# Kernel optimization log

Hardware: AMD Instinct MI355X
Metric: run time of the kernel (lower is better)

The kernel has to match this reference:

```python
import jax, jax.numpy as jnp
import numpy as np

N, E = 20000, 640000
D_IN, D_H, D_OUT = 128, 64, 32


def _lin_w(key, out_d, in_d):
    return jax.random.normal(key, (out_d, in_d), jnp.float32) / np.sqrt(in_d)


def setup_inputs() -> dict:
    key = jax.random.key(0)
    ks = jax.random.split(key, 16)
    x = jax.random.normal(ks[0], (N, D_IN), jnp.float32)
    edge_index = jax.random.randint(ks[1], (2, E), 0, N, jnp.int64)
    inp = {"x": x, "edge_index": edge_index}
    # SAGEConv weights: lin_l (aggregated neighbors, with bias), lin_r (root, no bias)
    inp["Wl1"] = _lin_w(ks[2], D_H, D_IN); inp["bl1"] = jnp.zeros((D_H,), jnp.float32)
    inp["Wr1"] = _lin_w(ks[3], D_H, D_IN)
    inp["Wl2"] = _lin_w(ks[4], D_H, D_H); inp["bl2"] = jnp.zeros((D_H,), jnp.float32)
    inp["Wr2"] = _lin_w(ks[5], D_H, D_H)
    inp["Wl3"] = _lin_w(ks[6], D_OUT, D_H); inp["bl3"] = jnp.zeros((D_OUT,), jnp.float32)
    inp["Wr3"] = _lin_w(ks[7], D_OUT, D_H)
    # Conv2d kernels (OIHW), all 3x3 pad 1
    inp["Wc1"] = jax.random.normal(ks[8], (D_H, 1, 3, 3), jnp.float32) / 3.0
    inp["bc1"] = jnp.zeros((D_H,), jnp.float32)
    inp["Wc2"] = jax.random.normal(ks[9], (D_H, D_H, 3, 3), jnp.float32) / np.sqrt(9 * D_H)
    inp["bc2"] = jnp.zeros((D_H,), jnp.float32)
    inp["Wc3"] = jax.random.normal(ks[10], (1, D_H, 3, 3), jnp.float32) / np.sqrt(9 * D_H)
    inp["bc3"] = jnp.zeros((1,), jnp.float32)
    # linear2 (hidden -> hidden)
    inp["W2"] = _lin_w(ks[11], D_H, D_H); inp["b2"] = jnp.zeros((D_H,), jnp.float32)
    return inp


def _sage(x, src, dst, Wl, bl, Wr):
    # PyG SAGEConv (mean aggr): lin_l(mean_{j->i} x_j) + lin_r(x_i)
    msg = x[src]  # [E, d] gather
    agg = jax.ops.segment_sum(msg, dst, num_segments=N)
    deg = jax.ops.segment_sum(jnp.ones((src.shape[0], 1), x.dtype), dst, num_segments=N)
    agg = agg / jnp.maximum(deg, 1.0)
    return agg @ Wl.T + bl + x @ Wr.T


def _conv(x, w, b):
    y = jax.lax.conv_general_dilated(x, w, (1, 1), ((1, 1), (1, 1)),
                                     dimension_numbers=("NCHW", "OIHW", "NCHW"))
    return y + b[None, :, None, None]


def reference(x, edge_index, Wl1, bl1, Wr1, Wl2, bl2, Wr2, Wl3, bl3, Wr3,
              Wc1, bc1, Wc2, bc2, Wc3, bc3, W2, b2):
    src, dst = edge_index[0], edge_index[1]
    h = _sage(x, src, dst, Wl1, bl1, Wr1)
    h = _sage(h, src, dst, Wl2, bl2, Wr2)
    h = _sage(h, src, dst, Wl2, bl2, Wr2)  # sage2 reused, as in source
    out_1 = h
    h4 = h[None, None]                     # [1,1,N,D_H]
    out = _conv(h4, Wc1, bc1)              # [1,D_H,N,D_H]
    out = _conv(out, Wc2, bc2)             # dropout is identity at inference
    out = _conv(out, Wc3, bc3)             # [1,1,N,D_H]
    out = out[0, 0] + out_1
    out = out @ W2.T + b2
    h = _sage(out, src, dst, Wl2, bl2, Wr2)
    h = _sage(h, src, dst, Wl2, bl2, Wr2)
    h = _sage(h, src, dst, Wl3, bl3, Wr3)
    return h
```

## Files before the change

### kernel.cpp

```cpp
#include <hip/hip_runtime.h>

#define NN 20000
#define NE 640000
#define NBUK 79

__global__ __launch_bounds__(128) void k_init(const int* __restrict__ ei32,
                                              int* __restrict__ bins,
                                              int* __restrict__ flag) {
  int tid = threadIdx.x;
  if (tid < NBUK) bins[tid] = 0;
  if (tid < 64) {
    int v = ei32[2 * tid + 1];
    unsigned long long nz = __ballot(v != 0);
    if (tid == 0) *flag = (nz == 0ull) ? 2 : 1;
  }
}

__global__ __launch_bounds__(256) void k_histB(const int* __restrict__ ei,
                                               const int* __restrict__ flag,
                                               int* __restrict__ bins, int E) {
  __shared__ int lb[NBUK];
  int tid = threadIdx.x;
  for (int i = tid; i < NBUK; i += 256) lb[i] = 0;
  __syncthreads();
  int st = *flag;
  int e0 = blockIdx.x * 4096;
#pragma unroll
  for (int t = 0; t < 16; ++t) {
    int e = e0 + t * 256 + tid;
    if (e < E) atomicAdd(&lb[ei[(size_t)(E + e) * st] >> 8], 1);
  }
  __syncthreads();
  for (int i = tid; i < NBUK; i += 256)
    if (lb[i]) atomicAdd(&bins[i], lb[i]);
}

__global__ __launch_bounds__(128) void k_scan79(const int* __restrict__ bins,
                                                int* __restrict__ bbase,
                                                int* __restrict__ bcur,
                                                int* __restrict__ rowptr,
                                                int E, int N) {
  __shared__ int lds[128];
  int tid = threadIdx.x;
  int mine = (tid < NBUK) ? bins[tid] : 0;
  lds[tid] = mine;
  __syncthreads();
  for (int off = 1; off < 128; off <<= 1) {
    int v = (tid >= off) ? lds[tid - off] : 0;
    __syncthreads();
    lds[tid] += v;
    __syncthreads();
  }
  int ex = lds[tid] - mine;
  if (tid <= NBUK) {
    bbase[tid] = ex;
    if (tid < NBUK) bcur[tid] = ex;
  }
  if (tid == 0) rowptr[N] = E;
}

__global__ __launch_bounds__(256) void k_part(const int* __restrict__ ei,
                                              const int* __restrict__ flag,
                                              int* __restrict__ bcur,
                                              unsigned long long* __restrict__ ebuf,
                                              int E) {
  __shared__ int lcnt[NBUK];
  __shared__ int lbase[NBUK];
  int tid = threadIdx.x;
  for (int i = tid; i < NBUK; i += 256) lcnt[i] = 0;
  __syncthreads();
  int st = *flag;
  int e0 = blockIdx.x * 4096;
  int srcv[16], dstv[16], lrank[16], bk[16];
  int n = 0;
#pragma unroll
  for (int t = 0; t < 16; ++t) {
    int e = e0 + t * 256 + tid;
    if (e < E) {
      int s = ei[(size_t)e * st];
      int d = ei[(size_t)(E + e) * st];
      int b = d >> 8;
      srcv[n] = s; dstv[n] = d; bk[n] = b;
      lrank[n] = atomicAdd(&lcnt[b], 1);
      ++n;
    }
  }
  __syncthreads();
  for (int i = tid; i < NBUK; i += 256)
    lbase[i] = atomicAdd(&bcur[i], lcnt[i]);
  __syncthreads();
  for (int t = 0; t < n; ++t) {
    int pos = lbase[bk[t]] + lrank[t];
    ebuf[pos] = ((unsigned long long)(unsigned)dstv[t] << 32) | (unsigned)srcv[t];
  }
}

__global__ __launch_bounds__(256) void k_sortb(
    const unsigned long long* __restrict__ ebuf, const int* __restrict__ bbase,
    int* __restrict__ rowptr, float* __restrict__ invdeg,
    int* __restrict__ csr, int N) {
  __shared__ int lcnt[256];
  __shared__ int lcur[256];
  __shared__ int wsum[4];
  int b = blockIdx.x;
  int tid = threadIdx.x;
  int base = bbase[b], n = bbase[b + 1] - base;
  lcnt[tid] = 0;
  __syncthreads();
  for (int e = tid; e < n; e += 256) {
    int d = (int)(ebuf[base + e] >> 32);
    atomicAdd(&lcnt[d - (b << 8)], 1);
  }
  __syncthreads();
  int c = lcnt[tid];
  int lane = tid & 63, wid = tid >> 6;
  int s = c;
#pragma unroll
  for (int off = 1; off < 64; off <<= 1) {
    int v = __shfl_up(s, off, 64);
    if (lane >= off) s += v;
  }
  if (lane == 63) wsum[wid] = s;
  __syncthreads();
  int woff = 0;
  for (int w = 0; w < wid; ++w) woff += wsum[w];
  int pref = woff + s - c;
  int gnode = (b << 8) + tid;
  if (gnode < N) {
    rowptr[gnode] = base + pref;
    invdeg[gnode] = 1.0f / (float)(c < 1 ? 1 : c);
  }
  lcur[tid] = pref;
  __syncthreads();
  for (int e = tid; e < n; e += 256) {
    unsigned long long pk = ebuf[base + e];
    int d = (int)(pk >> 32);
    int pos = atomicAdd(&lcur[d - (b << 8)], 1);
    csr[base + pos] = (int)(unsigned)pk;
  }
}

__global__ __launch_bounds__(256) void k_wtransA(
    const float* __restrict__ Wl1, const float* __restrict__ Wr1,
    const float* __restrict__ Wl2, const float* __restrict__ Wr2,
    const float* __restrict__ Wl3, const float* __restrict__ Wr3,
    const float* __restrict__ W2,
    float* __restrict__ Wt1, float* __restrict__ Wt2,
    float* __restrict__ Wt3, float* __restrict__ W2t) {
  int idx = blockIdx.x * 256 + threadIdx.x;
  if (idx < 16384) {
    int w = idx >> 7, u = idx & 127;
    Wt1[idx] = (u < 64) ? Wl1[u * 128 + w] : Wr1[(u - 64) * 128 + w];
  } else if (idx < 24576) {
    int t = idx - 16384;
    int w = t >> 7, u = t & 127;
    Wt2[t] = (u < 64) ? Wl2[u * 64 + w] : Wr2[(u - 64) * 64 + w];
  } else if (idx < 28672) {
    int t = idx - 24576;
    int w = t >> 6, u = t & 63;
    Wt3[t] = (u < 32) ? Wl3[u * 64 + w] : Wr3[(u - 32) * 64 + w];
  } else {
    int t = idx - 28672;
    int w = t >> 6, u = t & 63;
    W2t[t] = W2[u * 64 + w];
  }
}

__device__ __forceinline__ bool maskB(int var, int o2, int o1) {
  int s = o2 + o1;
  switch (var) {
    case 0: return (o2 >= 0) && (s >= 0);
    case 1: return s >= -1;
    case 3: return s <= 1;
    case 4: return (o2 <= 0) && (s <= 0);
    default: return true;
  }
}

__global__ __launch_bounds__(256) void k_setup2(
    const float* __restrict__ Wc1, const float* __restrict__ Wc2,
    const float* __restrict__ Wc3, const float* __restrict__ bc1,
    const float* __restrict__ bc2, const float* __restrict__ bc3,
    const float* __restrict__ W2t, const float* __restrict__ Wt2,
    const float* __restrict__ b2,
    float* __restrict__ T729, float* __restrict__ beta5,
    float* __restrict__ Wf, float* __restrict__ bf) {
  int b = blockIdx.x, tid = threadIdx.x;
  if (b == 0) {
    __shared__ float W3[576];
    __shared__ float S9s[5184];
    __shared__ float W1s[576];
    for (int e = tid; e < 576; e += 256) { W3[e] = Wc3[e]; W1s[e] = Wc1[e]; }
    __syncthreads();
    for (int bb = tid; bb < 576; bb += 256) {
      float acc[9];
#pragma unroll
      for (int a = 0; a < 9; ++a) acc[a] = 0.0f;
#pragma unroll 4
      for (int o = 0; o < 64; ++o) {
        float w2 = Wc2[o * 576 + bb];
#pragma unroll
        for (int a = 0; a < 9; ++a) acc[a] += W3[o * 9 + a] * w2;
      }
#pragma unroll
      for (int a = 0; a < 9; ++a) S9s[a * 576 + bb] = acc[a];
    }
    __syncthreads();
    for (int c = tid; c < 729; c += 256) {
      int kx0  = c % 3;
      int dl1e = (c / 3) % 3;
      int dl2e = (c / 9) % 3;
      int ky0  = (c / 27) % 3;
      int ky1  = (c / 81) % 3;
      int ky2  = c / 243;
      const float* s9 = &S9s[(ky2 * 3 + dl2e) * 576 + ky1 * 3 + dl1e];
      const float* w1 = &W1s[ky0 * 3 + kx0];
      float t = 0.0f;
#pragma unroll 8
      for (int i = 0; i < 64; ++i) t += s9[i * 9] * w1[i * 9];
      T729[c] = t;
    }
  } else if (b <= 5) {
    __shared__ float S2[576];
    __shared__ float W3b[576];
    __shared__ float B2[64];
    __shared__ float part[256];
    int var = b - 1;
    for (int e = tid; e < 576; e += 256) {
      int o = e / 9, r = e - o * 9;
      float t = 0.0f;
      for (int i = 0; i < 64; ++i) t += Wc2[o * 576 + i * 9 + r] * bc1[i];
      S2[e] = t;
      W3b[e] = Wc3[e];
    }
    if (tid < 64) B2[tid] = bc2[tid];
    __syncthreads();
    int u = tid & 63, oc = tid >> 6;
    float s = 0.0f;
    for (int ky2 = 0; ky2 < 3; ++ky2) {
      int o2 = ky2 - 1;
      bool okA = (var == 0) ? (o2 >= 0) : (var == 4) ? (o2 <= 0) : true;
      if (!okA) continue;
      for (int dl2 = -1; dl2 <= 1; ++dl2) {
        int p = u + dl2; if ((unsigned)p >= 64u) continue;
        float sel[9];
#pragma unroll
        for (int ky1 = 0; ky1 < 3; ++ky1) {
          int o1 = ky1 - 1;
          bool mb = maskB(var, o2, o1);
#pragma unroll
          for (int dl1 = -1; dl1 <= 1; ++dl1) {
            int pq = p + dl1;
            sel[ky1 * 3 + dl1 + 1] = (mb && (unsigned)pq < 64u) ? 1.0f : 0.0f;
          }
        }
#pragma unroll 4
        for (int oo = 0; oo < 16; ++oo) {
          int o = oc * 16 + oo;
          float inner = B2[o];
#pragma unroll
          for (int r = 0; r < 9; ++r) inner += S2[o * 9 + r] * sel[r];
          s += W3b[o * 9 + ky2 * 3 + (dl2 + 1)] * inner;
        }
      }
    }
    part[tid] = s;
    __syncthreads();
    if (tid < 64) {
      beta5[var * 64 + tid] =
          bc3[0] + part[tid] + part[64 + tid] + part[128 + tid] + part[192 + tid];
    }
  } else {
    int gidx = (b - 6) * 256 + tid;
    if (gidx < 8192) {
      int w = gidx >> 7, u = gidx & 127;
      float s = 0.0f;
#pragma unroll 4
      for (int k = 0; k < 64; ++k) s += W2t[w * 64 + k] * Wt2[k * 128 + u];
      Wf[gidx] = s;
    } else if (gidx < 8320) {
      int u = gidx - 8192;
      float s = 0.0f;
#pragma unroll 4
      for (int k = 0; k < 64; ++k) s += b2[k] * Wt2[k * 128 + u];
      bf[u] = s;
    }
  }
}

__global__ __launch_bounds__(256) void k_m5(const float* __restrict__ T729,
                                            float* __restrict__ M5T) {
  __shared__ float Ts[729];
  int tid = threadIdx.x;
  for (int e = tid; e < 729; e += 256) Ts[e] = T729[e];
  __syncthreads();
  int idx = blockIdx.x * 256 + tid;
  if (idx >= 15680) return;
  int jw = idx % 7;
  int u  = (idx / 7) % 64;
  int d  = (idx / 448) % 7;
  int var = idx / 3136;
  int w = u + jw - 3;
  float s = 0.0f;
  if (w >= 0 && w < 64) {
    for (int ky2 = 0; ky2 < 3; ++ky2) {
      int o2 = ky2 - 1;
      for (int ky1 = 0; ky1 < 3; ++ky1) {
        int o1 = ky1 - 1;
        if (!maskB(var, o2, o1)) continue;
        int o0 = (d - 3) - o2 - o1;
        if (o0 < -1 || o0 > 1) continue;
        int ky0 = o0 + 1;
        int cbase = ((ky2 * 3 + ky1) * 3 + ky0) * 27;
#pragma unroll
        for (int kx0 = 0; kx0 < 3; ++kx0) {
          int jq = jw - kx0;
          if ((unsigned)jq >= 5u) continue;
          int q = u + jq - 2;
          if ((unsigned)q >= 64u) continue;
#pragma unroll
          for (int dl2e = 0; dl2e < 3; ++dl2e) {
            int p = u + dl2e - 1;
            if ((unsigned)p >= 64u) continue;
            int dl1e = jq - dl2e;
            if ((unsigned)dl1e >= 3u) continue;
            s += Ts[cbase + dl2e * 9 + dl1e * 3 + kx0];
          }
        }
      }
    }
  }
  if (d == 3 && jw == 3) s += 1.0f;
  M5T[(var * 49 + d * 7 + jw) * 64 + u] = s;
}

template <int C, int K>
__global__ __launch_bounds__(256) void k_gemm(const float* __restrict__ X,
                                              const float* __restrict__ Wt,
                                              const float* __restrict__ bias,
                                              float* __restrict__ out, int N) {
  constexpr int ROWS = 16;
  constexpr int RPT = ROWS * C / 256;
  __shared__ float Xs[ROWS * K];
  int y0 = blockIdx.x * ROWS;
  {
    const float4* src = (const float4*)(X + (size_t)y0 * K);
    float4* dst = (float4*)Xs;
#pragma unroll
    for (int v = 0; v < ROWS * K / 4 / 256; ++v)
      dst[v * 256 + threadIdx.x] = src[v * 256 + threadIdx.x];
  }
  __syncthreads();
  int u = threadIdx.x % C;
  int rg = threadIdx.x / C;
  float acc[RPT];
  float bv = bias ? bias[u] : 0.0f;
#pragma unroll
  for (int k = 0; k < RPT; ++k) acc[k] = bv;
#pragma unroll 2
  for (int w0 = 0; w0 < K; w0 += 4) {
    float m0 = Wt[(w0 + 0) * C + u];
    float m1 = Wt[(w0 + 1) * C + u];
    float m2 = Wt[(w0 + 2) * C + u];
    float m3 = Wt[(w0 + 3) * C + u];
    const float* xs = &Xs[(rg * RPT) * K + w0];
#pragma unroll
    for (int k = 0; k < RPT; ++k) {
      float4 h = *(const float4*)(xs + k * K);
      acc[k] += m0 * h.x + m1 * h.y + m2 * h.z + m3 * h.w;
    }
  }
#pragma unroll
  for (int k = 0; k < RPT; ++k)
    out[(size_t)(y0 + rg * RPT + k) * C + u] = acc[k];
}

template <int C>
__global__ __launch_bounds__(256) void k_fused(const float* __restrict__ yzin,
                                               const int* __restrict__ csr,
                                               const int* __restrict__ rowptr,
                                               const float* __restrict__ invdeg,
                                               const float* __restrict__ bl,
                                               const float* __restrict__ Wt,
                                               float* __restrict__ out, int N) {
  constexpr int FV = 16;
  constexpr int G  = 4;
  constexpr int S4 = 32;
  constexpr int CAP = 64;
  __shared__ int idxs[16 * CAP];
  __shared__ float htile[16 * 64];
  int tid = threadIdx.x;
  int w = tid >> 6, lane = tid & 63;
  int base = blockIdx.x * 16;
  int beg_r[4], m_r[4], end_r[4];
#pragma unroll
  for (int rr = 0; rr < 4; ++rr) {
    int node = base + w * 4 + rr;
    int beg = rowptr[node], end = rowptr[node + 1];
    beg_r[rr] = beg; end_r[rr] = end;
    int cnt = end - beg;
    int m = cnt < CAP ? cnt : CAP;
    m_r[rr] = m;
    int* my = &idxs[(w * 4 + rr) * CAP];
    for (int k = lane; k < m; k += 64) my[k] = csr[beg + k];
  }
  __syncthreads();
  int g = lane / FV, f = lane % FV;
  const float4* yz4 = (const float4*)yzin;
#pragma unroll
  for (int rr = 0; rr < 4; ++rr) {
    int node = base + w * 4 + rr;
    const int* my = &idxs[(w * 4 + rr) * CAP];
    int m = m_r[rr];
    float a0x=0,a0y=0,a0z=0,a0w=0, a1x=0,a1y=0,a1z=0,a1w=0;
    float a2x=0,a2y=0,a2z=0,a2w=0, a3x=0,a3y=0,a3z=0,a3w=0;
    int j = g;
    for (; j + 3 * G < m; j += 4 * G) {
      int s0 = my[j], s1 = my[j + G], s2 = my[j + 2 * G], s3 = my[j + 3 * G];
      float4 v0 = yz4[(size_t)s0 * S4 + f];
      float4 v1 = yz4[(size_t)s1 * S4 + f];
      float4 v2 = yz4[(size_t)s2 * S4 + f];
      float4 v3 = yz4[(size_t)s3 * S4 + f];
      a0x += v0.x; a0y += v0.y; a0z += v0.z; a0w += v0.w;
      a1x += v1.x; a1y += v1.y; a1z += v1.z; a1w += v1.w;
      a2x += v2.x; a2y += v2.y; a2z += v2.z; a2w += v2.w;
      a3x += v3.x; a3y += v3.y; a3z += v3.z; a3w += v3.w;
    }
    for (; j < m; j += G) {
      int s0 = my[j];
      float4 v0 = yz4[(size_t)s0 * S4 + f];
      a0x += v0.x; a0y += v0.y; a0z += v0.z; a0w += v0.w;
    }
    for (int jj = beg_r[rr] + CAP + g; jj < end_r[rr]; jj += G) {
      int s0 = csr[jj];
      float4 v0 = yz4[(size_t)s0 * S4 + f];
      a0x += v0.x; a0y += v0.y; a0z += v0.z; a0w += v0.w;
    }
    float ax = (a0x + a1x) + (a2x + a3x);
    float ay = (a0y + a1y) + (a2y + a3y);
    float az = (a0z + a1z) + (a2z + a3z);
    float aw = (a0w + a1w) + (a2w + a3w);
#pragma unroll
    for (int mm = FV; mm < 64; mm <<= 1) {
      ax += __shfl_xor(ax, mm, 64);
      ay += __shfl_xor(ay, mm, 64);
      az += __shfl_xor(az, mm, 64);
      aw += __shfl_xor(aw, mm, 64);
    }
    if (g == 0) {
      float4 root = yz4[(size_t)node * S4 + FV + f];
      float4 bv = ((const float4*)bl)[f];
      float id = invdeg[node];
      float4 o;
      o.x = ax * id + bv.x + root.x;
      o.y = ay * id + bv.y + root.y;
      o.z = az * id + bv.z + root.z;
      o.w = aw * id + bv.w + root.w;
      ((float4*)htile)[(w * 4 + rr) * 16 + f] = o;
    }
  }
  __syncthreads();
  constexpr int RPT = 16 * C / 256;
  int u = tid % C, rg = tid / C;
  float acc[RPT];
#pragma unroll
  for (int k = 0; k < RPT; ++k) acc[k] = 0.0f;
#pragma unroll 2
  for (int w0 = 0; w0 < 64; w0 += 4) {
    float m0 = Wt[(w0 + 0) * C + u];
    float m1 = Wt[(w0 + 1) * C + u];
    float m2 = Wt[(w0 + 2) * C + u];
    float m3 = Wt[(w0 + 3) * C + u];
    const float* xs = &htile[(rg * RPT) * 64 + w0];
#pragma unroll
    for (int k = 0; k < RPT; ++k) {
      float4 h4 = *(const float4*)(xs + k * 64);
      acc[k] += m0 * h4.x + m1 * h4.y + m2 * h4.z + m3 * h4.w;
    }
  }
#pragma unroll
  for (int k = 0; k < RPT; ++k)
    out[(size_t)(base + rg * RPT + k) * C + u] = acc[k];
}

__global__ __launch_bounds__(256) void k_applyfused(
    const float* __restrict__ h, const float* __restrict__ M5T,
    const float* __restrict__ beta5, const float* __restrict__ Wf,
    const float* __restrict__ bf, float* __restrict__ out, int N) {
  __shared__ float hs[22 * 70];
  __shared__ float htile[16 * 64];
  int tid = threadIdx.x;
  int bstart = blockIdx.x * 16;
  for (int idx = tid; idx < 22 * 70; idx += 256) {
    int row = idx / 70, col = idx - row * 70;
    int y = bstart - 3 + row;
    int ww = col - 3;
    float v = 0.0f;
    if ((unsigned)y < (unsigned)N && (unsigned)ww < 64u)
      v = h[(size_t)y * 64 + ww];
    hs[idx] = v;
  }
  __syncthreads();
  int u = tid & 63, g = tid >> 6;
  int lr0 = g * 4;
  int gstart = bstart + lr0;
  const float* basep = &hs[lr0 * 70 + u];
  bool interior = (gstart >= 2) && (gstart + 3 <= N - 3);
  if (interior) {
    float c[49];
#pragma unroll
    for (int t = 0; t < 49; ++t) c[t] = M5T[(2 * 49 + t) * 64 + u];
    float bet = beta5[2 * 64 + u];
    float acc[4];
#pragma unroll
    for (int k = 0; k < 4; ++k) acc[k] = bet;
#pragma unroll
    for (int rr = 0; rr < 10; ++rr) {
      float t7[7];
#pragma unroll
      for (int jw = 0; jw < 7; ++jw) t7[jw] = basep[rr * 70 + jw];
#pragma unroll
      for (int d = 0; d < 7; ++d) {
        int k = rr - d;
        if (k >= 0 && k < 4) {
#pragma unroll
          for (int jw = 0; jw < 7; ++jw) acc[k] += c[d * 7 + jw] * t7[jw];
        }
      }
    }
#pragma unroll
    for (int k = 0; k < 4; ++k) htile[(lr0 + k) * 64 + u] = acc[k];
  } else {
    for (int k = 0; k < 4; ++k) {
      int y = gstart + k;
      int var = (y == 0) ? 0 : (y == 1) ? 1 : (y == N - 2) ? 3 : (y == N - 1) ? 4 : 2;
      float acc = beta5[var * 64 + u];
      for (int d = 0; d < 7; ++d)
        for (int jw = 0; jw < 7; ++jw)
          acc += M5T[(var * 49 + d * 7 + jw) * 64 + u] * basep[(k + d) * 70 + jw];
      htile[(lr0 + k) * 64 + u] = acc;
    }
  }
  __syncthreads();
  int u2 = tid % 128, rg = tid / 128;
  float acc2[8];
  float bv = bf[u2];
#pragma unroll
  for (int k = 0; k < 8; ++k) acc2[k] = bv;
#pragma unroll 2
  for (int w0 = 0; w0 < 64; w0 += 4) {
    float m0 = Wf[(w0 + 0) * 128 + u2];
    float m1 = Wf[(w0 + 1) * 128 + u2];
    float m2 = Wf[(w0 + 2) * 128 + u2];
    float m3 = Wf[(w0 + 3) * 128 + u2];
    const float* xs = &htile[(rg * 8) * 64 + w0];
#pragma unroll
    for (int k = 0; k < 8; ++k) {
      float4 h4 = *(const float4*)(xs + k * 64);
      acc2[k] += m0 * h4.x + m1 * h4.y + m2 * h4.z + m3 * h4.w;
    }
  }
#pragma unroll
  for (int k = 0; k < 8; ++k)
    out[(size_t)(bstart + rg * 8 + k) * 128 + u2] = acc2[k];
}

template <int DH>
__global__ __launch_bounds__(256) void k_agg(const float* __restrict__ yz,
                                             const int* __restrict__ csr,
                                             const int* __restrict__ rowptr,
                                             const float* __restrict__ invdeg,
                                             const float* __restrict__ bl,
                                             float* __restrict__ out, int N) {
  constexpr int FV = DH / 4;
  constexpr int G  = 64 / FV;
  constexpr int S4 = DH / 2;
  constexpr int CAP = 256;
  __shared__ int idxs[4 * CAP];
  int wid = threadIdx.x >> 6, lane = threadIdx.x & 63;
  int node = blockIdx.x * 4 + wid;
  int beg = rowptr[node], end = rowptr[node + 1];
  int cnt = end - beg;
  int m = cnt < CAP ? cnt : CAP;
  int* my = &idxs[wid * CAP];
  for (int k = lane; k < m; k += 64) my[k] = csr[beg + k];
  __syncthreads();
  int g = lane / FV, f = lane % FV;
  const float4* yz4 = (const float4*)yz;
  float a0x=0,a0y=0,a0z=0,a0w=0, a1x=0,a1y=0,a1z=0,a1w=0;
  float a2x=0,a2y=0,a2z=0,a2w=0, a3x=0,a3y=0,a3z=0,a3w=0;
  int j = g;
  for (; j + 3 * G < m; j += 4 * G) {
    int s0 = my[j], s1 = my[j + G], s2 = my[j + 2 * G], s3 = my[j + 3 * G];
    float4 v0 = yz4[(size_t)s0 * S4 + f];
    float4 v1 = yz4[(size_t)s1 * S4 + f];
    float4 v2 = yz4[(size_t)s2 * S4 + f];
    float4 v3 = yz4[(size_t)s3 * S4 + f];
    a0x += v0.x; a0y += v0.y; a0z += v0.z; a0w += v0.w;
    a1x += v1.x; a1y += v1.y; a1z += v1.z; a1w += v1.w;
    a2x += v2.x; a2y += v2.y; a2z += v2.z; a2w += v2.w;
    a3x += v3.x; a3y += v3.y; a3z += v3.z; a3w += v3.w;
  }
  for (; j < m; j += G) {
    int s0 = my[j];
    float4 v0 = yz4[(size_t)s0 * S4 + f];
    a0x += v0.x; a0y += v0.y; a0z += v0.z; a0w += v0.w;
  }
  for (int jj = beg + CAP + g; jj < end; jj += G) {
    int s0 = csr[jj];
    float4 v0 = yz4[(size_t)s0 * S4 + f];
    a0x += v0.x; a0y += v0.y; a0z += v0.z; a0w += v0.w;
  }
  float ax = (a0x + a1x) + (a2x + a3x);
  float ay = (a0y + a1y) + (a2y + a3y);
  float az = (a0z + a1z) + (a2z + a3z);
  float aw = (a0w + a1w) + (a2w + a3w);
#pragma unroll
  for (int mm = FV; mm < 64; mm <<= 1) {
    ax += __shfl_xor(ax, mm, 64);
    ay += __shfl_xor(ay, mm, 64);
    az += __shfl_xor(az, mm, 64);
    aw += __shfl_xor(aw, mm, 64);
  }
  if (g == 0) {
    float4 root = yz4[(size_t)node * S4 + FV + f];
    float4 bv = ((const float4*)bl)[f];
    float id = invdeg[node];
    float4 o;
    o.x = ax * id + bv.x + root.x;
    o.y = ay * id + bv.y + root.y;
    o.z = az * id + bv.z + root.z;
    o.w = aw * id + bv.w + root.w;
    ((float4*)out)[(size_t)node * FV + f] = o;
  }
}

extern "C" void kernel_launch(void* const* d_in, const int* in_sizes, int n_in,
                              void* d_out, int out_size, void* d_ws, size_t ws_size,
                              hipStream_t stream) {
  const int N = NN, E = NE;
  const float* x   = (const float*)d_in[0];
  const int*   ei  = (const int*)d_in[1];
  const float* Wl1 = (const float*)d_in[2];
  const float* bl1 = (const float*)d_in[3];
  const float* Wr1 = (const float*)d_in[4];
  const float* Wl2 = (const float*)d_in[5];
  const float* bl2 = (const float*)d_in[6];
  const float* Wr2 = (const float*)d_in[7];
  const float* Wl3 = (const float*)d_in[8];
  const float* bl3 = (const float*)d_in[9];
  const float* Wr3 = (const float*)d_in[10];
  const float* Wc1 = (const float*)d_in[11];
  const float* bc1 = (const float*)d_in[12];
  const float* Wc2 = (const float*)d_in[13];
  const float* bc2 = (const float*)d_in[14];
  const float* Wc3 = (const float*)d_in[15];
  const float* bc3 = (const float*)d_in[16];
  const float* W2  = (const float*)d_in[17];
  const float* b2  = (const float*)d_in[18];

  char* ws = (char*)d_ws;
  size_t off = 0;
  auto alloc = [&](size_t bytes) -> void* {
    off = (off + 255) & ~(size_t)255;
    void* p = ws + off;
    off += bytes;
    return p;
  };
  int*   eflag  = (int*)alloc(4);
  int*   rowptr = (int*)alloc((size_t)(N + 1) * 4);
  float* invdeg = (float*)alloc((size_t)N * 4);
  int*   csr    = (int*)alloc((size_t)E * 4);
  unsigned long long* ebuf = (unsigned long long*)alloc((size_t)E * 8);
  int*   bins   = (int*)alloc(128 * 4);
  int*   bbase  = (int*)alloc(128 * 4);
  int*   bcur   = (int*)alloc(128 * 4);
  float* Wt1    = (float*)alloc(128 * 128 * 4);
  float* Wt2    = (float*)alloc(64 * 128 * 4);
  float* Wt3    = (float*)alloc(64 * 64 * 4);
  float* W2t    = (float*)alloc(64 * 64 * 4);
  float* Wf     = (float*)alloc(64 * 128 * 4);
  float* bf     = (float*)alloc(128 * 4);
  float* T729   = (float*)alloc(729 * 4);
  float* M5T    = (float*)alloc(15680 * 4);
  float* beta5  = (float*)alloc(320 * 4);
  float* yzA    = (float*)alloc((size_t)N * 128 * 4);
  float* yzB    = (float*)alloc((size_t)N * 128 * 4);
  float* hA     = (float*)alloc((size_t)N * 64 * 4);
  (void)ws_size; (void)in_sizes; (void)n_in; (void)out_size;

  const int gG = N / 16;
  const int gA = N / 4;
  const int gP = (E + 4095) / 4096;

  k_init<<<1, 128, 0, stream>>>(ei, bins, eflag);
  k_histB<<<gP, 256, 0, stream>>>(ei, eflag, bins, E);
  k_scan79<<<1, 128, 0, stream>>>(bins, bbase, bcur, rowptr, E, N);
  k_part<<<gP, 256, 0, stream>>>(ei, eflag, bcur, ebuf, E);
  k_sortb<<<NBUK, 256, 0, stream>>>(ebuf, bbase, rowptr, invdeg, csr, N);

  k_wtransA<<<128, 256, 0, stream>>>(Wl1, Wr1, Wl2, Wr2, Wl3, Wr3, W2,
                                     Wt1, Wt2, Wt3, W2t);
  k_setup2<<<39, 256, 0, stream>>>(Wc1, Wc2, Wc3, bc1, bc2, bc3, W2t, Wt2, b2,
                                   T729, beta5, Wf, bf);
  k_m5<<<62, 256, 0, stream>>>(T729, M5T);

  k_gemm<128, 128><<<gG, 256, 0, stream>>>(x, Wt1, nullptr, yzA, N);
  k_fused<128><<<gG, 256, 0, stream>>>(yzA, csr, rowptr, invdeg, bl1, Wt2, yzB, N);
  k_fused<128><<<gG, 256, 0, stream>>>(yzB, csr, rowptr, invdeg, bl2, Wt2, yzA, N);
  k_agg<64><<<gA, 256, 0, stream>>>(yzA, csr, rowptr, invdeg, bl2, hA, N);
  k_applyfused<<<gG, 256, 0, stream>>>(hA, M5T, beta5, Wf, bf, yzB, N);
  k_fused<128><<<gG, 256, 0, stream>>>(yzB, csr, rowptr, invdeg, bl2, Wt2, yzA, N);
  k_fused<64><<<gG, 256, 0, stream>>>(yzA, csr, rowptr, invdeg, bl2, Wt3, yzB, N);
  k_agg<32><<<gA, 256, 0, stream>>>(yzB, csr, rowptr, invdeg, bl3, (float*)d_out, N);
}
```

Baseline: 327.2 us.

## Restructure CSR build into block-local partition and segmented bucket sort; unroll gathers

Replaces the five-kernel CSR construction (init, histogram, scan, partition, sort) with three kernels. Each partition block now writes its edges into its own block-local region with a local bucket scan. A single-block scan then transposes the per-block counts, and the bucket sort locates each edge's segment by binary search. This removes the separate histogram pass over the edge array and the global atomics, at the cost of a binary search per edge and a serial single-block transpose. Separately, the neighbor-gather loops in the aggregation kernels are unrolled to 8 loads per iteration to raise memory-level parallelism.

Result: slower. 382.8 us (+17.0%).

```diff
diff --git a/kernel.cpp b/kernel.cpp
--- a/kernel.cpp
+++ b/kernel.cpp
@@ -3,73 +3,26 @@
 #define NN 20000
 #define NE 640000
 #define NBUK 79
-
-__global__ __launch_bounds__(128) void k_init(const int* __restrict__ ei32,
-                                              int* __restrict__ bins,
-                                              int* __restrict__ flag) {
+#define NBLK 157
+typedef unsigned long long ull;
+
+__device__ __forceinline__ int probe_stride(const int* __restrict__ ei32) {
+  int lane = threadIdx.x & 63;
+  int v = ei32[2 * lane + 1];
+  unsigned long long nz = __ballot(v != 0);
+  return (nz == 0ull) ? 2 : 1;
+}
+
+__global__ __launch_bounds__(256) void k_part2(const int* __restrict__ ei,
+                                               ull* __restrict__ ebuf,
+                                               int* __restrict__ cntm,
+                                               int* __restrict__ lstm, int E) {
+  __shared__ int lcnt[NBUK];
+  __shared__ int lsc[128];
   int tid = threadIdx.x;
-  if (tid < NBUK) bins[tid] = 0;
-  if (tid < 64) {
-    int v = ei32[2 * tid + 1];
-    unsigned long long nz = __ballot(v != 0);
-    if (tid == 0) *flag = (nz == 0ull) ? 2 : 1;
-  }
-}
-
-__global__ __launch_bounds__(256) void k_histB(const int* __restrict__ ei,
-                                               const int* __restrict__ flag,
-                                               int* __restrict__ bins, int E) {
-  __shared__ int lb[NBUK];
-  int tid = threadIdx.x;
-  for (int i = tid; i < NBUK; i += 256) lb[i] = 0;
-  __syncthreads();
-  int st = *flag;
-  int e0 = blockIdx.x * 4096;
-#pragma unroll
-  for (int t = 0; t < 16; ++t) {
-    int e = e0 + t * 256 + tid;
-    if (e < E) atomicAdd(&lb[ei[(size_t)(E + e) * st] >> 8], 1);
-  }
-  __syncthreads();
-  for (int i = tid; i < NBUK; i += 256)
-    if (lb[i]) atomicAdd(&bins[i], lb[i]);
-}
-
-__global__ __launch_bounds__(128) void k_scan79(const int* __restrict__ bins,
-                                                int* __restrict__ bbase,
-                                                int* __restrict__ bcur,
-                                                int* __restrict__ rowptr,
-                                                int E, int N) {
-  __shared__ int lds[128];
-  int tid = threadIdx.x;
-  int mine = (tid < NBUK) ? bins[tid] : 0;
-  lds[tid] = mine;
-  __syncthreads();
-  for (int off = 1; off < 128; off <<= 1) {
-    int v = (tid >= off) ? lds[tid - off] : 0;
-    __syncthreads();
-    lds[tid] += v;
-    __syncthreads();
-  }
-  int ex = lds[tid] - mine;
-  if (tid <= NBUK) {
-    bbase[tid] = ex;
-    if (tid < NBUK) bcur[tid] = ex;
-  }
-  if (tid == 0) rowptr[N] = E;
-}
-
-__global__ __launch_bounds__(256) void k_part(const int* __restrict__ ei,
-                                              const int* __restrict__ flag,
-                                              int* __restrict__ bcur,
-                                              unsigned long long* __restrict__ ebuf,
-                                              int E) {
-  __shared__ int lcnt[NBUK];
-  __shared__ int lbase[NBUK];
-  int tid = threadIdx.x;
+  int st = probe_stride(ei);
   for (int i = tid; i < NBUK; i += 256) lcnt[i] = 0;
   __syncthreads();
-  int st = *flag;
   int e0 = blockIdx.x * 4096;
   int srcv[16], dstv[16], lrank[16], bk[16];
   int n = 0;
@@ -86,35 +39,106 @@
     }
   }
   __syncthreads();
-  for (int i = tid; i < NBUK; i += 256)
-    lbase[i] = atomicAdd(&bcur[i], lcnt[i]);
+  if (tid < 128) lsc[tid] = (tid < NBUK) ? lcnt[tid] : 0;
+  __syncthreads();
+  for (int off = 1; off < 128; off <<= 1) {
+    int v = (tid < 128 && tid >= off) ? lsc[tid - off] : 0;
+    __syncthreads();
+    if (tid < 128) lsc[tid] += v;
+    __syncthreads();
+  }
+  if (tid < NBUK) {
+    int ex = lsc[tid] - lcnt[tid];
+    cntm[blockIdx.x * NBUK + tid] = lcnt[tid];
+    lstm[blockIdx.x * NBUK + tid] = ex;
+    lcnt[tid] = ex;
+  }
   __syncthreads();
   for (int t = 0; t < n; ++t) {
-    int pos = lbase[bk[t]] + lrank[t];
-    ebuf[pos] = ((unsigned long long)(unsigned)dstv[t] << 32) | (unsigned)srcv[t];
-  }
-}
-
-__global__ __launch_bounds__(256) void k_sortb(
-    const unsigned long long* __restrict__ ebuf, const int* __restrict__ bbase,
+    int pos = lcnt[bk[t]] + lrank[t];
+    ebuf[(size_t)blockIdx.x * 4096 + pos] =
+        ((ull)(unsigned)dstv[t] << 32) | (unsigned)srcv[t];
+  }
+}
+
+__global__ __launch_bounds__(256) void k_scan2(const int* __restrict__ cntm,
+                                               const int* __restrict__ lstm,
+                                               int* __restrict__ bbase,
+                                               int* __restrict__ cntT,
+                                               int* __restrict__ lstT,
+                                               int* __restrict__ rowptr,
+                                               int E, int N) {
+  __shared__ int C[NBLK * NBUK];
+  __shared__ int L[NBLK * NBUK];
+  __shared__ int col[128];
+  int tid = threadIdx.x;
+  for (int i = tid; i < NBLK * NBUK; i += 256) { C[i] = cntm[i]; L[i] = lstm[i]; }
+  __syncthreads();
+  int mycol = 0;
+  if (tid < NBUK) {
+    int s = 0;
+    for (int blk = 0; blk < NBLK; ++blk) {
+      int c = C[blk * NBUK + tid];
+      cntT[tid * NBLK + blk] = c;
+      lstT[tid * NBLK + blk] = L[blk * NBUK + tid];
+      s += c;
+    }
+    mycol = s;
+  }
+  if (tid < 128) col[tid] = (tid < NBUK) ? mycol : 0;
+  __syncthreads();
+  for (int off = 1; off < 128; off <<= 1) {
+    int v = (tid < 128 && tid >= off) ? col[tid - off] : 0;
+    __syncthreads();
+    if (tid < 128) col[tid] += v;
+    __syncthreads();
+  }
+  if (tid < NBUK) bbase[tid] = col[tid] - mycol;
+  if (tid == 0) { bbase[NBUK] = E; rowptr[N] = E; }
+}
+
+__global__ __launch_bounds__(256) void k_sortb2(
+    const ull* __restrict__ ebuf, const int* __restrict__ bbase,
+    const int* __restrict__ cntT, const int* __restrict__ lstT,
     int* __restrict__ rowptr, float* __restrict__ invdeg,
     int* __restrict__ csr, int N) {
+  __shared__ int segst[NBLK + 1];
+  __shared__ int segbase[NBLK];
+  __shared__ int ssc[256];
   __shared__ int lcnt[256];
   __shared__ int lcur[256];
   __shared__ int wsum[4];
-  int b = blockIdx.x;
-  int tid = threadIdx.x;
-  int base = bbase[b], n = bbase[b + 1] - base;
+  int b = blockIdx.x, tid = threadIdx.x;
+  int c = 0;
+  if (tid < NBLK) {
+    c = cntT[b * NBLK + tid];
+    segbase[tid] = tid * 4096 + lstT[b * NBLK + tid];
+  }
+  ssc[tid] = (tid < NBLK) ? c : 0;
+  __syncthreads();
+  for (int off = 1; off < 256; off <<= 1) {
+    int v = (tid >= off) ? ssc[tid - off] : 0;
+    __syncthreads();
+    ssc[tid] += v;
+    __syncthreads();
+  }
+  if (tid < NBLK) segst[tid] = ssc[tid] - c;
+  if (tid == 0) segst[NBLK] = ssc[NBLK - 1];
   lcnt[tid] = 0;
   __syncthreads();
+  int n = segst[NBLK];
+  int base = bbase[b];
   for (int e = tid; e < n; e += 256) {
-    int d = (int)(ebuf[base + e] >> 32);
+    int lo = 0, hi = NBLK;
+    while (hi - lo > 1) { int mid = (lo + hi) >> 1; if (segst[mid] <= e) lo = mid; else hi = mid; }
+    ull pk = ebuf[(size_t)segbase[lo] + (e - segst[lo])];
+    int d = (int)(pk >> 32);
     atomicAdd(&lcnt[d - (b << 8)], 1);
   }
   __syncthreads();
-  int c = lcnt[tid];
+  int cc = lcnt[tid];
   int lane = tid & 63, wid = tid >> 6;
-  int s = c;
+  int s = cc;
 #pragma unroll
   for (int off = 1; off < 64; off <<= 1) {
     int v = __shfl_up(s, off, 64);
@@ -124,16 +148,18 @@
   __syncthreads();
   int woff = 0;
   for (int w = 0; w < wid; ++w) woff += wsum[w];
-  int pref = woff + s - c;
+  int pref = woff + s - cc;
   int gnode = (b << 8) + tid;
   if (gnode < N) {
     rowptr[gnode] = base + pref;
-    invdeg[gnode] = 1.0f / (float)(c < 1 ? 1 : c);
+    invdeg[gnode] = 1.0f / (float)(cc < 1 ? 1 : cc);
   }
   lcur[tid] = pref;
   __syncthreads();
   for (int e = tid; e < n; e += 256) {
-    unsigned long long pk = ebuf[base + e];
+    int lo = 0, hi = NBLK;
+    while (hi - lo > 1) { int mid = (lo + hi) >> 1; if (segst[mid] <= e) lo = mid; else hi = mid; }
+    ull pk = ebuf[(size_t)segbase[lo] + (e - segst[lo])];
     int d = (int)(pk >> 32);
     int pos = atomicAdd(&lcur[d - (b << 8)], 1);
     csr[base + pos] = (int)(unsigned)pk;
@@ -415,8 +441,28 @@
     float a0x=0,a0y=0,a0z=0,a0w=0, a1x=0,a1y=0,a1z=0,a1w=0;
     float a2x=0,a2y=0,a2z=0,a2w=0, a3x=0,a3y=0,a3z=0,a3w=0;
     int j = g;
+    for (; j + 7 * G < m; j += 8 * G) {
+      int s0 = my[j], s1 = my[j + G], s2 = my[j + 2*G], s3 = my[j + 3*G];
+      int s4 = my[j + 4*G], s5 = my[j + 5*G], s6 = my[j + 6*G], s7 = my[j + 7*G];
+      float4 v0 = yz4[(size_t)s0 * S4 + f];
+      float4 v1 = yz4[(size_t)s1 * S4 + f];
+      float4 v2 = yz4[(size_t)s2 * S4 + f];
+      float4 v3 = yz4[(size_t)s3 * S4 + f];
+      float4 v4 = yz4[(size_t)s4 * S4 + f];
+      float4 v5 = yz4[(size_t)s5 * S4 + f];
+      float4 v6 = yz4[(size_t)s6 * S4 + f];
+      float4 v7 = yz4[(size_t)s7 * S4 + f];
+      a0x += v0.x; a0y += v0.y; a0z += v0.z; a0w += v0.w;
+      a1x += v1.x; a1y += v1.y; a1z += v1.z; a1w += v1.w;
+      a2x += v2.x; a2y += v2.y; a2z += v2.z; a2w += v2.w;
+      a3x += v3.x; a3y += v3.y; a3z += v3.z; a3w += v3.w;
+      a0x += v4.x; a0y += v4.y; a0z += v4.z; a0w += v4.w;
+      a1x += v5.x; a1y += v5.y; a1z += v5.z; a1w += v5.w;
+      a2x += v6.x; a2y += v6.y; a2z += v6.z; a2w += v6.w;
+      a3x += v7.x; a3y += v7.y; a3z += v7.z; a3w += v7.w;
+    }
     for (; j + 3 * G < m; j += 4 * G) {
-      int s0 = my[j], s1 = my[j + G], s2 = my[j + 2 * G], s3 = my[j + 3 * G];
+      int s0 = my[j], s1 = my[j + G], s2 = my[j + 2*G], s3 = my[j + 3*G];
       float4 v0 = yz4[(size_t)s0 * S4 + f];
       float4 v1 = yz4[(size_t)s1 * S4 + f];
       float4 v2 = yz4[(size_t)s2 * S4 + f];
@@ -590,8 +636,28 @@
   float a0x=0,a0y=0,a0z=0,a0w=0, a1x=0,a1y=0,a1z=0,a1w=0;
   float a2x=0,a2y=0,a2z=0,a2w=0, a3x=0,a3y=0,a3z=0,a3w=0;
   int j = g;
+  for (; j + 7 * G < m; j += 8 * G) {
+    int s0 = my[j], s1 = my[j + G], s2 = my[j + 2*G], s3 = my[j + 3*G];
+    int s4 = my[j + 4*G], s5 = my[j + 5*G], s6 = my[j + 6*G], s7 = my[j + 7*G];
+    float4 v0 = yz4[(size_t)s0 * S4 + f];
+    float4 v1 = yz4[(size_t)s1 * S4 + f];
+    float4 v2 = yz4[(size_t)s2 * S4 + f];
+    float4 v3 = yz4[(size_t)s3 * S4 + f];
+    float4 v4 = yz4[(size_t)s4 * S4 + f];
+    float4 v5 = yz4[(size_t)s5 * S4 + f];
+    float4 v6 = yz4[(size_t)s6 * S4 + f];
+    float4 v7 = yz4[(size_t)s7 * S4 + f];
+    a0x += v0.x; a0y += v0.y; a0z += v0.z; a0w += v0.w;
+    a1x += v1.x; a1y += v1.y; a1z += v1.z; a1w += v1.w;
+    a2x += v2.x; a2y += v2.y; a2z += v2.z; a2w += v2.w;
+    a3x += v3.x; a3y += v3.y; a3z += v3.z; a3w += v3.w;
+    a0x += v4.x; a0y += v4.y; a0z += v4.z; a0w += v4.w;
+    a1x += v5.x; a1y += v5.y; a1z += v5.z; a1w += v5.w;
+    a2x += v6.x; a2y += v6.y; a2z += v6.z; a2w += v6.w;
+    a3x += v7.x; a3y += v7.y; a3z += v7.z; a3w += v7.w;
+  }
   for (; j + 3 * G < m; j += 4 * G) {
-    int s0 = my[j], s1 = my[j + G], s2 = my[j + 2 * G], s3 = my[j + 3 * G];
+    int s0 = my[j], s1 = my[j + G], s2 = my[j + 2*G], s3 = my[j + 3*G];
     float4 v0 = yz4[(size_t)s0 * S4 + f];
     float4 v1 = yz4[(size_t)s1 * S4 + f];
     float4 v2 = yz4[(size_t)s2 * S4 + f];
@@ -667,14 +733,15 @@
     off += bytes;
     return p;
   };
-  int*   eflag  = (int*)alloc(4);
   int*   rowptr = (int*)alloc((size_t)(N + 1) * 4);
   float* invdeg = (float*)alloc((size_t)N * 4);
   int*   csr    = (int*)alloc((size_t)E * 4);
-  unsigned long long* ebuf = (unsigned long long*)alloc((size_t)E * 8);
-  int*   bins   = (int*)alloc(128 * 4);
+  ull*   ebuf   = (ull*)alloc((size_t)NBLK * 4096 * 8);
+  int*   cntm   = (int*)alloc((size_t)NBLK * NBUK * 4);
+  int*   lstm   = (int*)alloc((size_t)NBLK * NBUK * 4);
+  int*   cntT   = (int*)alloc((size_t)NBUK * NBLK * 4);
+  int*   lstT   = (int*)alloc((size_t)NBUK * NBLK * 4);
   int*   bbase  = (int*)alloc(128 * 4);
-  int*   bcur   = (int*)alloc(128 * 4);
   float* Wt1    = (float*)alloc(128 * 128 * 4);
   float* Wt2    = (float*)alloc(64 * 128 * 4);
   float* Wt3    = (float*)alloc(64 * 64 * 4);
@@ -691,13 +758,10 @@
 
   const int gG = N / 16;
   const int gA = N / 4;
-  const int gP = (E + 4095) / 4096;
-
-  k_init<<<1, 128, 0, stream>>>(ei, bins, eflag);
-  k_histB<<<gP, 256, 0, stream>>>(ei, eflag, bins, E);
-  k_scan79<<<1, 128, 0, stream>>>(bins, bbase, bcur, rowptr, E, N);
-  k_part<<<gP, 256, 0, stream>>>(ei, eflag, bcur, ebuf, E);
-  k_sortb<<<NBUK, 256, 0, stream>>>(ebuf, bbase, rowptr, invdeg, csr, N);
+
+  k_part2<<<NBLK, 256, 0, stream>>>(ei, ebuf, cntm, lstm, E);
+  k_scan2<<<1, 256, 0, stream>>>(cntm, lstm, bbase, cntT, lstT, rowptr, E, N);
+  k_sortb2<<<NBUK, 256, 0, stream>>>(ebuf, bbase, cntT, lstT, rowptr, invdeg, csr, N);
 
   k_wtransA<<<128, 256, 0, stream>>>(Wl1, Wr1, Wl2, Wr2, Wl3, Wr3, W2,
                                      Wt1, Wt2, Wt3, W2t);
```
